# Kernel tuning notes

Measured on AMD Instinct MI355X. Metric: run time of the kernel, lower is better.

## Reference

```python
import jax, jax.numpy as jnp
import numpy as np

B, L, D_IN, H, FEAT, PROJ = 1024, 128, 130, 768, 49, 40


def setup_inputs() -> dict:
    key = jax.random.key(0)
    ks = jax.random.split(key, 16)
    s = 0.05
    return {
        "X": jax.random.normal(ks[0], (B, L, D_IN), dtype=jnp.float32),
        "Fe": jax.random.normal(ks[1], (B, FEAT), dtype=jnp.float32),
        # three attention heads densa1/2/3 stacked: [3, H, L]
        "W_att": jax.random.normal(ks[2], (3, H, L), dtype=jnp.float32) * s,
        "b_att": jax.random.normal(ks[3], (3, L), dtype=jnp.float32) * s,
        # LSTMCell(3*D_IN, H) params, PyTorch layout
        "W_ih": jax.random.normal(ks[4], (4 * H, 3 * D_IN), dtype=jnp.float32) * s,
        "W_hh": jax.random.normal(ks[5], (4 * H, H), dtype=jnp.float32) * s,
        "b_ih": jax.random.normal(ks[6], (4 * H,), dtype=jnp.float32) * s,
        "b_hh": jax.random.normal(ks[7], (4 * H,), dtype=jnp.float32) * s,
        # Dense1: Linear(H, FEAT)
        "W_d1": jax.random.normal(ks[8], (FEAT, H), dtype=jnp.float32) * s,
        "b_d1": jax.random.normal(ks[9], (FEAT,), dtype=jnp.float32) * s,
        # AttFeat R: Linear(FEAT, PROJ); A: Linear(PROJ, 1, bias=False)
        "W_r": jax.random.normal(ks[10], (PROJ, FEAT), dtype=jnp.float32) * s,
        "b_r": jax.random.normal(ks[11], (PROJ,), dtype=jnp.float32) * s,
        "W_a": jax.random.normal(ks[12], (1, PROJ), dtype=jnp.float32) * s,
        # Dense2: Linear(PROJ, 2)
        "W_d2": jax.random.normal(ks[13], (2, PROJ), dtype=jnp.float32) * s,
        "b_d2": jax.random.normal(ks[14], (2,), dtype=jnp.float32) * s,
    }


def reference(X, Fe, W_att, b_att, W_ih, W_hh, b_ih, b_hh, W_d1, b_d1, W_r, b_r, W_a, W_d2, b_d2):
    b = X.shape[0]

    def step(carry, _):
        h, c = carry
        # three softmax attention distributions over the sequence: [b, 3, L]
        logits = jnp.einsum('bh,khl->bkl', h, W_att) + b_att
        alp = jax.nn.softmax(logits, axis=-1)
        # weighted sums over seq -> concat of v1,v2,v3: [b, 3*D_IN]
        v = jnp.einsum('bkl,bld->bkd', alp, X).reshape(b, -1)
        # PyTorch LSTMCell update
        gates = v @ W_ih.T + b_ih + h @ W_hh.T + b_hh
        i, f, g, o = jnp.split(gates, 4, axis=-1)
        c_new = jax.nn.sigmoid(f) * c + jax.nn.sigmoid(i) * jnp.tanh(g)
        h_new = jax.nn.sigmoid(o) * jnp.tanh(c_new)
        return (h_new, c_new), h_new

    h0 = jnp.zeros((b, H), dtype=X.dtype)
    c0 = jnp.zeros((b, H), dtype=X.dtype)
    _, hs = jax.lax.scan(step, (h0, c0), None, length=L)  # [L, b, H]
    out = jnp.transpose(hs, (1, 0, 2))                    # [b, L, H]

    # MaxLayer: max-pool over the sequence dim
    x = jnp.max(out, axis=1)                              # [b, H]

    # Dense1 + ReLU
    y = jax.nn.relu(x @ W_d1.T + b_d1)                    # [b, FEAT]

    # AttFeat over [y, Fe]
    r1 = jax.nn.leaky_relu(y @ W_r.T + b_r)               # [b, PROJ]
    r2 = jax.nn.leaky_relu(Fe @ W_r.T + b_r)
    a1 = jnp.tanh(r1) @ W_a.T                             # [b, 1]
    a2 = jnp.tanh(r2) @ W_a.T
    a = jax.nn.softmax(jnp.concatenate([a1, a2], axis=-1), axis=-1)  # [b, 2]
    s = jax.nn.relu(a[:, 0:1] * r1 + a[:, 1:2] * r2)      # [b, PROJ]

    # Dense2 (squeeze is a no-op for b > 1)
    return s @ W_d2.T + b_d2                              # [b, 2]
```

## Files before the change

kernel.cpp:

```cpp
#include <hip/hip_runtime.h>
#include <stdint.h>


#define B_SZ   1024
#define LSEQ   128
#define DIN    130
#define HDIM   768
#define NFEAT  49
#define NPROJ  40
#define KPAD   1216
#define VOFF   416
#define NGATE  3072
#define KT_G   19
#define XELEM  (LSEQ * DIN)
#define GBUF   28672

typedef unsigned short u16;
typedef __attribute__((ext_vector_type(8))) short short8;
typedef __attribute__((ext_vector_type(4))) float f32x4;

__device__ __forceinline__ u16 f2bf(float f) {
  unsigned int u = __float_as_uint(f);
  u += 0x7FFFu + ((u >> 16) & 1u);
  return (u16)(u >> 16);
}
__device__ __forceinline__ float bf2f(u16 b) {
  return __uint_as_float(((unsigned int)b) << 16);
}
__device__ __forceinline__ float frcp(float x) {
  return __builtin_amdgcn_rcpf(x);
}
__device__ __forceinline__ float ftanh(float x) {
  return 1.f - 2.f * frcp(1.f + __expf(2.f * x));
}
__device__ __forceinline__ float fsigm(float x) {
  return frcp(1.f + __expf(-x));
}
__device__ __forceinline__ void gload16(const void* g, void* l) {
  __builtin_amdgcn_global_load_lds(
      (__attribute__((address_space(1))) const void*)g,
      (__attribute__((address_space(3))) void*)l, 16, 0, 0);
}

__global__ __launch_bounds__(256, 4) void gemm_logits_k(
    const u16* __restrict__ Ah,
    const u16* __restrict__ Bh, float* __restrict__ Cp)
{
  __shared__ __align__(16) u16 sAh[32 * 40];
  __shared__ __align__(16) u16 sBh[64 * 40];

  const int tid = threadIdx.x, lane = tid & 63, wid = tid >> 6;
  const int wm = (wid & 1) * 16, wn = (wid >> 1) * 32;
  const int lm = lane & 15, quad = lane >> 4;
  const int bm = blockIdx.x * 32, bn = blockIdx.y * 64;
  const int kh = blockIdx.z;
  const int kbase = kh * 384;
  float* __restrict__ C = Cp + (size_t)kh * B_SZ * 384;

  const bool aload = tid < 128;
  const int ar = tid >> 2, ac = (tid & 3) * 8;
  const size_t a_off = (size_t)(bm + ar) * KPAD + kbase + ac;
  const size_t b_off = (size_t)(bn + ar) * HDIM + kbase + ac;

  uint4 ph, pb;
  if (aload) ph = *(const uint4*)(Ah + a_off);
  pb = *(const uint4*)(Bh + b_off);

  f32x4 acc0 = {0.f, 0.f, 0.f, 0.f}, acc1 = {0.f, 0.f, 0.f, 0.f};

  for (int kt = 0; kt < 12; ++kt) {
    if (aload) *(uint4*)&sAh[ar * 40 + ac] = ph;
    *(uint4*)&sBh[ar * 40 + ac] = pb;
    __syncthreads();
    if (kt + 1 < 12) {
      const int k0 = (kt + 1) * 32;
      if (aload) ph = *(const uint4*)(Ah + a_off + k0);
      pb = *(const uint4*)(Bh + b_off + k0);
    }
    const short8 ah = *(const short8*)&sAh[(wm + lm) * 40 + quad * 8];
    const short8 b0 = *(const short8*)&sBh[(wn + lm) * 40 + quad * 8];
    const short8 b1 = *(const short8*)&sBh[(wn + 16 + lm) * 40 + quad * 8];
    acc0 = __builtin_amdgcn_mfma_f32_16x16x32_bf16(ah, b0, acc0, 0, 0, 0);
    acc1 = __builtin_amdgcn_mfma_f32_16x16x32_bf16(ah, b1, acc1, 0, 0, 0);
    __syncthreads();
  }

  const int col = bn + wn + lm;
  const int row0 = bm + wm + quad * 4;
#pragma unroll
  for (int r = 0; r < 4; ++r) {
    C[(size_t)(row0 + r) * 384 + col]      = acc0[r];
    C[(size_t)(row0 + r) * 384 + col + 16] = acc1[r];
  }
}

__global__ __launch_bounds__(512, 2) void gates_lstm(
    const u16* __restrict__ Ah,
    const u16* __restrict__ Wh,
    const float* __restrict__ bsum,
    float* __restrict__ cst, float* __restrict__ hmax,
    u16* __restrict__ out_h)
{
  __shared__ __align__(16) char smem[2 * GBUF];

  const int tid = threadIdx.x, lane = tid & 63, wid = tid >> 6;
  const int wm = (wid >> 1) * 32, wn = (wid & 1) * 48;
  const int lm = lane & 15, quad = lane >> 4;

  const int wg = blockIdx.x;
  const int vid = (wg & 7) * 32 + (wg >> 3);
  const int bm = (vid & 7) * 128;
  const int j0 = (vid >> 3) * 24;

  const u16* Asrc[2];
#pragma unroll
  for (int i = 0; i < 2; ++i) {
    const int r = i * 64 + (tid >> 3);
    const int s = (tid & 7) ^ (r & 7);
    Asrc[i] = Ah + (size_t)(bm + r) * KPAD + (s << 3);
  }
  const u16* Bsrc0;
  const u16* Bsrc1;
  {
    const int r0 = tid >> 3;
    const int s0 = (tid & 7) ^ (r0 & 7);
    const int nrow0 = (r0 / 24) * HDIM + j0 + (r0 % 24);
    Bsrc0 = Wh + (size_t)nrow0 * KPAD + (s0 << 3);
    const int r1 = 64 + (tid >> 3);
    const int s1 = (tid & 7) ^ (r1 & 7);
    const int r1c = (r1 < 96) ? r1 : 95;
    const int nrow1 = (r1c / 24) * HDIM + j0 + (r1c % 24);
    Bsrc1 = Wh + (size_t)nrow1 * KPAD + (s1 << 3);
  }

  int aoff[2], boff[3];
#pragma unroll
  for (int mi = 0; mi < 2; ++mi) {
    const int R = wm + mi * 16 + lm;
    aoff[mi] = R * 64 + ((quad ^ (R & 7)) << 3);
  }
#pragma unroll
  for (int ni = 0; ni < 3; ++ni) {
    const int R = wn + ni * 16 + lm;
    boff[ni] = R * 64 + ((quad ^ (R & 7)) << 3);
  }

  f32x4 acc[2][3];
#pragma unroll
  for (int mi = 0; mi < 2; ++mi)
#pragma unroll
    for (int ni = 0; ni < 3; ++ni) acc[mi][ni] = (f32x4){0.f, 0.f, 0.f, 0.f};

  auto stage = [&](int buf, int kt) {
    char* bb = smem + buf * GBUF;
    const int k0 = kt * 64;
    gload16(Asrc[0] + k0, bb + (tid << 4));
    gload16(Asrc[1] + k0, bb + 8192 + (tid << 4));
    gload16(Bsrc0 + k0, bb + 16384 + (tid << 4));
    if (tid < 256)
      gload16(Bsrc1 + k0, bb + 24576 + (tid << 4));
  };

  stage(0, 0);

  for (int kt = 0; kt < KT_G; ++kt) {
    if (kt + 1 < KT_G) {
      stage((kt + 1) & 1, kt + 1);
      if (wid < 4) asm volatile("s_waitcnt vmcnt(4)" ::: "memory");
      else         asm volatile("s_waitcnt vmcnt(3)" ::: "memory");
    } else {
      asm volatile("s_waitcnt vmcnt(0)" ::: "memory");
    }
    asm volatile("s_barrier" ::: "memory");

    const u16* sA = (const u16*)(smem + (kt & 1) * GBUF);
    const u16* sB = sA + 8192;
#pragma unroll
    for (int kk = 0; kk < 2; ++kk) {
      const int kx = kk << 5;
      short8 af[2], bg[3];
#pragma unroll
      for (int mi = 0; mi < 2; ++mi)
        af[mi] = *(const short8*)(sA + (aoff[mi] ^ kx));
#pragma unroll
      for (int ni = 0; ni < 3; ++ni)
        bg[ni] = *(const short8*)(sB + (boff[ni] ^ kx));
#pragma unroll
      for (int mi = 0; mi < 2; ++mi)
#pragma unroll
        for (int ni = 0; ni < 3; ++ni)
          acc[mi][ni] = __builtin_amdgcn_mfma_f32_16x16x32_bf16(
              af[mi], bg[ni], acc[mi][ni], 0, 0, 0);
    }
    asm volatile("s_barrier" ::: "memory");
  }

  float* tile = (float*)smem;
#pragma unroll
  for (int mi = 0; mi < 2; ++mi)
#pragma unroll
    for (int ni = 0; ni < 3; ++ni) {
      const int c = wn + ni * 16 + lm;
#pragma unroll
      for (int r = 0; r < 4; ++r)
        tile[(wm + mi * 16 + quad * 4 + r) * 100 + c] = acc[mi][ni][r];
    }
  __syncthreads();

#pragma unroll
  for (int i = 0; i < 6; ++i) {
    const int lin = tid + 512 * i;
    const int row = lin / 24, jj = lin - row * 24;
    const int b = bm + row, j = j0 + jj;
    const float* tr = tile + row * 100;
    const float pi = tr[jj]      + bsum[j];
    const float pf = tr[24 + jj] + bsum[HDIM + j];
    const float pg = tr[48 + jj] + bsum[2 * HDIM + j];
    const float po = tr[72 + jj] + bsum[3 * HDIM + j];
    const float si = fsigm(pi);
    const float sf = fsigm(pf);
    const float so = fsigm(po);
    const size_t cidx = (size_t)b * HDIM + j;
    const float cn = sf * cst[cidx] + si * ftanh(pg);
    const float hn = so * ftanh(cn);
    cst[cidx] = cn;
    hmax[cidx] = fmaxf(hmax[cidx], hn);
    out_h[(size_t)b * KPAD + VOFF + j] = f2bf(hn);
  }
}

__global__ __launch_bounds__(512, 4) void softmax_v(
    const float* __restrict__ l0, const float* __restrict__ l1,
    const float* __restrict__ b_att,
    const u16* __restrict__ XT,
    u16* __restrict__ act)
{
  const int b = blockIdx.x;
  const int t = threadIdx.x;
  __shared__ __align__(16) u16 sXT[XELEM];
  __shared__ __align__(16) float s_alp[384];
  __shared__ float s_w[16];

  {
    const uint4* src = (const uint4*)(XT + (size_t)b * XELEM);
    uint4* dst = (uint4*)sXT;
#pragma unroll
    for (int rep = 0; rep < 4; ++rep) {
      const int i = t + rep * 512;
      const int d = i >> 4, blk = i & 15;
      dst[d * 16 + (blk ^ (d & 7))] = src[i];
    }
    if (t < 32) {
      const int i = 2048 + t;
      const int d = i >> 4, blk = i & 15;
      dst[d * 16 + (blk ^ (d & 7))] = src[i];
    }
  }

  const int lane = t & 63, wv = t >> 6, hw = wv & ~1;
  float x = -3.4e38f;
  if (t < 384)
    x = l0[(size_t)b * 384 + t] + l1[(size_t)b * 384 + t] + b_att[t];

  float m = x;
#pragma unroll
  for (int off = 32; off > 0; off >>= 1) m = fmaxf(m, __shfl_xor(m, off));
  if (lane == 0 && wv < 6) s_w[wv] = m;
  __syncthreads();

  float e = 0.f;
  if (t < 384) e = __expf(x - fmaxf(s_w[hw], s_w[hw | 1]));
  float sum = e;
#pragma unroll
  for (int off = 32; off > 0; off >>= 1) sum += __shfl_xor(sum, off);
  if (lane == 0 && wv < 6) s_w[8 + wv] = sum;
  __syncthreads();

  if (t < 384) {
    const float sk = s_w[8 + hw] + s_w[8 + (hw | 1)];
    s_alp[t] = e * frcp(sk);
  }
  __syncthreads();

  if (t < 390) {
    const int k = t / 130;
    const int d = t - k * 130;
    const uint4* xr = (const uint4*)sXT;
    const int dbase = d * 16, dsw = d & 7;
    const float* ab = s_alp + (k << 7);
    float acc = 0.f;
#pragma unroll
    for (int c = 0; c < 16; ++c) {
      const uint4 raw = xr[dbase + (c ^ dsw)];
      const float4 a0 = *(const float4*)(ab + (c << 3));
      const float4 a1 = *(const float4*)(ab + (c << 3) + 4);
      acc += a0.x * bf2f((u16)(raw.x & 0xffff));
      acc += a0.y * bf2f((u16)(raw.x >> 16));
      acc += a0.z * bf2f((u16)(raw.y & 0xffff));
      acc += a0.w * bf2f((u16)(raw.y >> 16));
      acc += a1.x * bf2f((u16)(raw.z & 0xffff));
      acc += a1.y * bf2f((u16)(raw.z >> 16));
      acc += a1.z * bf2f((u16)(raw.w & 0xffff));
      acc += a1.w * bf2f((u16)(raw.w >> 16));
    }
    act[(size_t)b * KPAD + t] = f2bf(acc);
  }
}

__global__ __launch_bounds__(64) void final_head(
    const float* __restrict__ hmax, const float* __restrict__ Fe,
    const float* __restrict__ W_d1, const float* __restrict__ b_d1,
    const float* __restrict__ W_r,  const float* __restrict__ b_r,
    const float* __restrict__ W_a,
    const float* __restrict__ W_d2, const float* __restrict__ b_d2,
    float* __restrict__ out)
{
  const int b = blockIdx.x;
  const int t = threadIdx.x;
  __shared__ float sx[HDIM];
  __shared__ float sy[NFEAT];
  __shared__ float sr1[NPROJ], sr2[NPROJ];
  __shared__ float sa[2];

  for (int i = t; i < HDIM; i += 64) sx[i] = hmax[(size_t)b * HDIM + i];
  __syncthreads();

  if (t < NFEAT) {
    float acc = b_d1[t];
    const float* w = W_d1 + (size_t)t * HDIM;
    for (int i = 0; i < HDIM; ++i) acc += sx[i] * w[i];
    sy[t] = fmaxf(acc, 0.f);
  }
  __syncthreads();

  if (t < NPROJ) {
    float a1 = b_r[t], a2 = b_r[t];
    const float* w  = W_r + (size_t)t * NFEAT;
    const float* fe = Fe + (size_t)b * NFEAT;
    for (int i = 0; i < NFEAT; ++i) { a1 += sy[i] * w[i]; a2 += fe[i] * w[i]; }
    sr1[t] = (a1 > 0.f) ? a1 : 0.01f * a1;
    sr2[t] = (a2 > 0.f) ? a2 : 0.01f * a2;
  }
  __syncthreads();

  if (t == 0) {
    float a1 = 0.f, a2 = 0.f;
    for (int p = 0; p < NPROJ; ++p) {
      a1 += tanhf(sr1[p]) * W_a[p];
      a2 += tanhf(sr2[p]) * W_a[p];
    }
    const float mx = fmaxf(a1, a2);
    const float e1 = expf(a1 - mx), e2 = expf(a2 - mx);
    sa[0] = e1 / (e1 + e2);
    sa[1] = e2 / (e1 + e2);
  }
  __syncthreads();

  if (t < 2) {
    float acc = b_d2[t];
    const float* w = W_d2 + (size_t)t * NPROJ;
    for (int p = 0; p < NPROJ; ++p) {
      float s = sa[0] * sr1[p] + sa[1] * sr2[p];
      s = fmaxf(s, 0.f);
      acc += s * w[p];
    }
    out[(size_t)b * 2 + t] = acc;
  }
}

__global__ __launch_bounds__(256) void pack_w(
    const float* __restrict__ W_ih, const float* __restrict__ W_hh,
    const float* __restrict__ b_ih, const float* __restrict__ b_hh,
    u16* __restrict__ hi, float* __restrict__ bsum)
{
  const int idx = blockIdx.x * 256 + threadIdx.x;
  if (idx >= NGATE * KPAD) return;
  const int n = idx / KPAD;
  const int k = idx - n * KPAD;
  float v = 0.f;
  if (k < 3 * DIN)                       v = W_ih[(size_t)n * (3 * DIN) + k];
  else if (k >= VOFF && k < VOFF + HDIM) v = W_hh[(size_t)n * HDIM + (k - VOFF)];
  hi[idx] = f2bf(v);
  if (k == 0) bsum[n] = b_ih[n] + b_hh[n];
}

__global__ __launch_bounds__(256) void pack_watt(
    const float* __restrict__ W_att,
    u16* __restrict__ hi)
{
  const int idx = blockIdx.x * 256 + threadIdx.x;
  if (idx >= 384 * HDIM) return;
  const int n = idx / HDIM;
  const int h = idx - n * HDIM;
  const int katt = n >> 7;
  const int l = n & 127;
  hi[idx] = f2bf(W_att[((size_t)katt * HDIM + h) * LSEQ + l]);
}

__global__ __launch_bounds__(256) void pack_xt(
    const float* __restrict__ X, u16* __restrict__ XT)
{
  const int b = blockIdx.x;
  const int t = threadIdx.x;
  __shared__ u16 sX[XELEM];
  const float* src = X + (size_t)b * XELEM;
  for (int i = t; i < XELEM; i += 256) sX[i] = f2bf(src[i]);
  __syncthreads();
  uint4* dst = (uint4*)(XT + (size_t)b * XELEM);
  for (int u = t; u < 2080; u += 256) {
    const int d = u >> 4, blk = u & 15;
    const int lb = blk * 8;
    ushort4 w0, w1;
    w0.x = sX[(lb + 0) * DIN + d]; w0.y = sX[(lb + 1) * DIN + d];
    w0.z = sX[(lb + 2) * DIN + d]; w0.w = sX[(lb + 3) * DIN + d];
    w1.x = sX[(lb + 4) * DIN + d]; w1.y = sX[(lb + 5) * DIN + d];
    w1.z = sX[(lb + 6) * DIN + d]; w1.w = sX[(lb + 7) * DIN + d];
    uint4 o;
    o.x = (unsigned)w0.x | ((unsigned)w0.y << 16);
    o.y = (unsigned)w0.z | ((unsigned)w0.w << 16);
    o.z = (unsigned)w1.x | ((unsigned)w1.y << 16);
    o.w = (unsigned)w1.z | ((unsigned)w1.w << 16);
    dst[u] = o;
  }
}

__global__ __launch_bounds__(256) void init_state(
    u16* __restrict__ a0, u16* __restrict__ a1,
    float* __restrict__ cst, float* __restrict__ hmax)
{
  const int idx = blockIdx.x * 256 + threadIdx.x;
  if (idx < B_SZ * KPAD) { a0[idx] = 0; a1[idx] = 0; }
  if (idx < B_SZ * HDIM) { cst[idx] = 0.f; hmax[idx] = -3.4e38f; }
}

extern "C" void kernel_launch(void* const* d_in, const int* in_sizes, int n_in,
                              void* d_out, int out_size, void* d_ws, size_t ws_size,
                              hipStream_t stream) {
  const float* X     = (const float*)d_in[0];
  const float* Fe    = (const float*)d_in[1];
  const float* W_att = (const float*)d_in[2];
  const float* b_att = (const float*)d_in[3];
  const float* W_ih  = (const float*)d_in[4];
  const float* W_hh  = (const float*)d_in[5];
  const float* b_ih  = (const float*)d_in[6];
  const float* b_hh  = (const float*)d_in[7];
  const float* W_d1  = (const float*)d_in[8];
  const float* b_d1  = (const float*)d_in[9];
  const float* W_r   = (const float*)d_in[10];
  const float* b_r   = (const float*)d_in[11];
  const float* W_a   = (const float*)d_in[12];
  const float* W_d2  = (const float*)d_in[13];
  const float* b_d2  = (const float*)d_in[14];
  float* out = (float*)d_out;

  char* base = (char*)d_ws;
  size_t off = 0;
  auto alloc = [&](size_t nbytes) -> void* {
    void* p = base + off;
    off = (off + nbytes + 255) & ~(size_t)255;
    return p;
  };
  u16* act0    = (u16*)alloc((size_t)B_SZ * KPAD * 2);
  u16* act1    = (u16*)alloc((size_t)B_SZ * KPAD * 2);
  u16* wcat    = (u16*)alloc((size_t)NGATE * KPAD * 2);
  u16* watt    = (u16*)alloc((size_t)384 * HDIM * 2);
  u16* xt16    = (u16*)alloc((size_t)B_SZ * XELEM * 2);
  float* bsum  = (float*)alloc((size_t)NGATE * 4);
  float* lpart = (float*)alloc((size_t)2 * B_SZ * 384 * 4);
  float* cst   = (float*)alloc((size_t)B_SZ * HDIM * 4);
  float* hmax  = (float*)alloc((size_t)B_SZ * HDIM * 4);

  pack_w<<<(NGATE * KPAD + 255) / 256, 256, 0, stream>>>(W_ih, W_hh, b_ih, b_hh, wcat, bsum);
  pack_watt<<<(384 * HDIM + 255) / 256, 256, 0, stream>>>(W_att, watt);
  pack_xt<<<B_SZ, 256, 0, stream>>>(X, xt16);
  init_state<<<(B_SZ * KPAD + 255) / 256, 256, 0, stream>>>(act0, act1, cst, hmax);

  float* l0 = lpart;
  float* l1 = lpart + (size_t)B_SZ * 384;

  gemm_logits_k<<<dim3(B_SZ / 32, 384 / 64, 2), 256, 0, stream>>>(act0 + VOFF, watt, lpart);
  softmax_v<<<B_SZ, 512, 0, stream>>>(l0, l1, b_att, xt16, act0);

  u16 *rd = act0, *wr = act1;
  for (int step = 0; step < LSEQ; ++step) {
    gates_lstm<<<dim3(256), 512, 0, stream>>>(rd, wcat, bsum, cst, hmax, wr);
    if (step + 1 < LSEQ) {
      gemm_logits_k<<<dim3(B_SZ / 32, 384 / 64, 2), 256, 0, stream>>>(wr + VOFF, watt, lpart);
      softmax_v<<<B_SZ, 512, 0, stream>>>(l0, l1, b_att, xt16, wr);
    }
    u16* tt = rd; rd = wr; wr = tt;
  }

  final_head<<<B_SZ, 64, 0, stream>>>(hmax, Fe, W_d1, b_d1, W_r, b_r, W_a, W_d2, b_d2, out);
}
```

Before: 4.089 ms.

## Split K across warps in gates GEMM and halve logits GEMM N-tile

The gates_lstm kernel now assigns each warp a 64x48 output tile over one half of each 64-wide K slice, and two warps split K. Their partial accumulators are summed through shared memory in two phases. Each warp issues fewer LDS fragment loads per MFMA, at the cost of more accumulator registers and an extra barrier plus read-modify-write in the epilogue. The logits GEMM switches from 32x64 to 32x32 tiles with one MFMA per warp, doubling the grid so more blocks are in flight, but each block does less work.

```diff
diff --git a/kernel.cpp b/kernel.cpp
--- a/kernel.cpp
+++ b/kernel.cpp
@@ -47,51 +47,47 @@
     const u16* __restrict__ Bh, float* __restrict__ Cp)
 {
   __shared__ __align__(16) u16 sAh[32 * 40];
-  __shared__ __align__(16) u16 sBh[64 * 40];
+  __shared__ __align__(16) u16 sBh[32 * 40];
 
   const int tid = threadIdx.x, lane = tid & 63, wid = tid >> 6;
-  const int wm = (wid & 1) * 16, wn = (wid >> 1) * 32;
+  const int wm = (wid & 1) * 16, wn = (wid >> 1) * 16;
   const int lm = lane & 15, quad = lane >> 4;
-  const int bm = blockIdx.x * 32, bn = blockIdx.y * 64;
+  const int bm = blockIdx.x * 32, bn = blockIdx.y * 32;
   const int kh = blockIdx.z;
   const int kbase = kh * 384;
   float* __restrict__ C = Cp + (size_t)kh * B_SZ * 384;
 
   const bool aload = tid < 128;
-  const int ar = tid >> 2, ac = (tid & 3) * 8;
+  const int ar = (tid & 127) >> 2, ac = (tid & 3) * 8;
   const size_t a_off = (size_t)(bm + ar) * KPAD + kbase + ac;
   const size_t b_off = (size_t)(bn + ar) * HDIM + kbase + ac;
 
-  uint4 ph, pb;
-  if (aload) ph = *(const uint4*)(Ah + a_off);
-  pb = *(const uint4*)(Bh + b_off);
-
-  f32x4 acc0 = {0.f, 0.f, 0.f, 0.f}, acc1 = {0.f, 0.f, 0.f, 0.f};
+  uint4 p;
+  if (aload) p = *(const uint4*)(Ah + a_off);
+  else       p = *(const uint4*)(Bh + b_off);
+
+  f32x4 acc = {0.f, 0.f, 0.f, 0.f};
 
   for (int kt = 0; kt < 12; ++kt) {
-    if (aload) *(uint4*)&sAh[ar * 40 + ac] = ph;
-    *(uint4*)&sBh[ar * 40 + ac] = pb;
+    if (aload) *(uint4*)&sAh[ar * 40 + ac] = p;
+    else       *(uint4*)&sBh[ar * 40 + ac] = p;
     __syncthreads();
     if (kt + 1 < 12) {
       const int k0 = (kt + 1) * 32;
-      if (aload) ph = *(const uint4*)(Ah + a_off + k0);
-      pb = *(const uint4*)(Bh + b_off + k0);
+      if (aload) p = *(const uint4*)(Ah + a_off + k0);
+      else       p = *(const uint4*)(Bh + b_off + k0);
     }
     const short8 ah = *(const short8*)&sAh[(wm + lm) * 40 + quad * 8];
     const short8 b0 = *(const short8*)&sBh[(wn + lm) * 40 + quad * 8];
-    const short8 b1 = *(const short8*)&sBh[(wn + 16 + lm) * 40 + quad * 8];
-    acc0 = __builtin_amdgcn_mfma_f32_16x16x32_bf16(ah, b0, acc0, 0, 0, 0);
-    acc1 = __builtin_amdgcn_mfma_f32_16x16x32_bf16(ah, b1, acc1, 0, 0, 0);
+    acc = __builtin_amdgcn_mfma_f32_16x16x32_bf16(ah, b0, acc, 0, 0, 0);
     __syncthreads();
   }
 
   const int col = bn + wn + lm;
   const int row0 = bm + wm + quad * 4;
 #pragma unroll
-  for (int r = 0; r < 4; ++r) {
-    C[(size_t)(row0 + r) * 384 + col]      = acc0[r];
-    C[(size_t)(row0 + r) * 384 + col + 16] = acc1[r];
-  }
+  for (int r = 0; r < 4; ++r)
+    C[(size_t)(row0 + r) * 384 + col] = acc[r];
 }
 
 __global__ __launch_bounds__(512, 2) void gates_lstm(
@@ -104,7 +100,9 @@
   __shared__ __align__(16) char smem[2 * GBUF];
 
   const int tid = threadIdx.x, lane = tid & 63, wid = tid >> 6;
-  const int wm = (wid >> 1) * 32, wn = (wid & 1) * 48;
+  const int wm = (wid >> 2) * 64;
+  const int wn = ((wid >> 1) & 1) * 48;
+  const int kw = wid & 1;
   const int lm = lane & 15, quad = lane >> 4;
 
   const int wg = blockIdx.x;
@@ -133,21 +131,21 @@
     Bsrc1 = Wh + (size_t)nrow1 * KPAD + (s1 << 3);
   }
 
-  int aoff[2], boff[3];
-#pragma unroll
-  for (int mi = 0; mi < 2; ++mi) {
+  int aoffk[4], boffk[3];
+#pragma unroll
+  for (int mi = 0; mi < 4; ++mi) {
     const int R = wm + mi * 16 + lm;
-    aoff[mi] = R * 64 + ((quad ^ (R & 7)) << 3);
+    aoffk[mi] = (R * 64 + ((quad ^ (R & 7)) << 3)) ^ (kw << 5);
   }
 #pragma unroll
   for (int ni = 0; ni < 3; ++ni) {
     const int R = wn + ni * 16 + lm;
-    boff[ni] = R * 64 + ((quad ^ (R & 7)) << 3);
-  }
-
-  f32x4 acc[2][3];
-#pragma unroll
-  for (int mi = 0; mi < 2; ++mi)
+    boffk[ni] = (R * 64 + ((quad ^ (R & 7)) << 3)) ^ (kw << 5);
+  }
+
+  f32x4 acc[4][3];
+#pragma unroll
+  for (int mi = 0; mi < 4; ++mi)
 #pragma unroll
     for (int ni = 0; ni < 3; ++ni) acc[mi][ni] = (f32x4){0.f, 0.f, 0.f, 0.f};
 
@@ -175,36 +173,47 @@
 
     const u16* sA = (const u16*)(smem + (kt & 1) * GBUF);
     const u16* sB = sA + 8192;
-#pragma unroll
-    for (int kk = 0; kk < 2; ++kk) {
-      const int kx = kk << 5;
-      short8 af[2], bg[3];
-#pragma unroll
-      for (int mi = 0; mi < 2; ++mi)
-        af[mi] = *(const short8*)(sA + (aoff[mi] ^ kx));
+    short8 af[4], bg[3];
+#pragma unroll
+    for (int mi = 0; mi < 4; ++mi)
+      af[mi] = *(const short8*)(sA + aoffk[mi]);
+#pragma unroll
+    for (int ni = 0; ni < 3; ++ni)
+      bg[ni] = *(const short8*)(sB + boffk[ni]);
+#pragma unroll
+    for (int mi = 0; mi < 4; ++mi)
 #pragma unroll
       for (int ni = 0; ni < 3; ++ni)
-        bg[ni] = *(const short8*)(sB + (boff[ni] ^ kx));
-#pragma unroll
-      for (int mi = 0; mi < 2; ++mi)
-#pragma unroll
-        for (int ni = 0; ni < 3; ++ni)
-          acc[mi][ni] = __builtin_amdgcn_mfma_f32_16x16x32_bf16(
-              af[mi], bg[ni], acc[mi][ni], 0, 0, 0);
-    }
+        acc[mi][ni] = __builtin_amdgcn_mfma_f32_16x16x32_bf16(
+            af[mi], bg[ni], acc[mi][ni], 0, 0, 0);
+
     asm volatile("s_barrier" ::: "memory");
   }
 
   float* tile = (float*)smem;
-#pragma unroll
-  for (int mi = 0; mi < 2; ++mi)
-#pragma unroll
-    for (int ni = 0; ni < 3; ++ni) {
-      const int c = wn + ni * 16 + lm;
-#pragma unroll
-      for (int r = 0; r < 4; ++r)
-        tile[(wm + mi * 16 + quad * 4 + r) * 100 + c] = acc[mi][ni][r];
-    }
+  if (kw == 0) {
+#pragma unroll
+    for (int mi = 0; mi < 4; ++mi)
+#pragma unroll
+      for (int ni = 0; ni < 3; ++ni) {
+        const int c = wn + ni * 16 + lm;
+#pragma unroll
+        for (int r = 0; r < 4; ++r)
+          tile[(wm + mi * 16 + quad * 4 + r) * 100 + c] = acc[mi][ni][r];
+      }
+  }
+  __syncthreads();
+  if (kw == 1) {
+#pragma unroll
+    for (int mi = 0; mi < 4; ++mi)
+#pragma unroll
+      for (int ni = 0; ni < 3; ++ni) {
+        const int c = wn + ni * 16 + lm;
+#pragma unroll
+        for (int r = 0; r < 4; ++r)
+          tile[(wm + mi * 16 + quad * 4 + r) * 100 + c] += acc[mi][ni][r];
+      }
+  }
   __syncthreads();
 
 #pragma unroll
@@ -478,14 +487,14 @@
   float* l0 = lpart;
   float* l1 = lpart + (size_t)B_SZ * 384;
 
-  gemm_logits_k<<<dim3(B_SZ / 32, 384 / 64, 2), 256, 0, stream>>>(act0 + VOFF, watt, lpart);
+  gemm_logits_k<<<dim3(B_SZ / 32, 384 / 32, 2), 256, 0, stream>>>(act0 + VOFF, watt, lpart);
   softmax_v<<<B_SZ, 512, 0, stream>>>(l0, l1, b_att, xt16, act0);
 
   u16 *rd = act0, *wr = act1;
   for (int step = 0; step < LSEQ; ++step) {
     gates_lstm<<<dim3(256), 512, 0, stream>>>(rd, wcat, bsum, cst, hmax, wr);
     if (step + 1 < LSEQ) {
-      gemm_logits_k<<<dim3(B_SZ / 32, 384 / 64, 2), 256, 0, stream>>>(wr + VOFF, watt, lpart);
+      gemm_logits_k<<<dim3(B_SZ / 32, 384 / 32, 2), 256, 0, stream>>>(wr + VOFF, watt, lpart);
       softmax_v<<<B_SZ, 512, 0, stream>>>(l0, l1, b_att, xt16, wr);
     }
     u16* tt = rd; rd = wr; wr = tt;
```

After: 4.192 ms. +2.5%, slower.
